# Kernel optimization log

Hardware: AMD Instinct MI355X
Metric: run time of the kernel (lower is better)

Reference implementation:

```python
import jax, jax.numpy as jnp
import numpy as np

N, NFEAT, NHID, NHEADS, NCLASS, NBLOCKS = 4096, 1024, 64, 8, 8, 3
ALPHA = 0.1       # LeakyReLU negative slope
NEG = -9e15       # mask value used by pyGAT


def setup_inputs() -> dict:
    key = jax.random.key(0)
    ks = jax.random.split(key, 8)
    x = jax.random.normal(ks[0], (N, NFEAT), jnp.float32)
    # sparse-ish symmetric adjacency with self loops (0/1 int mask)
    a = (jax.random.uniform(ks[1], (N, N)) < 0.01).astype(jnp.int32)
    adj = jnp.maximum(jnp.maximum(a, a.T), jnp.eye(N, dtype=jnp.int32))
    s = 0.1
    W_heads = (jax.random.normal(ks[2], (NHEADS, NFEAT, NHID), jnp.float32) * s)
    a_heads = (jax.random.normal(ks[3], (NHEADS, 2 * NHID), jnp.float32) * s)
    W_out = (jax.random.normal(ks[4], (NHEADS * NHID, NHID), jnp.float32) * s)
    a_out = (jax.random.normal(ks[5], (2 * NHID,), jnp.float32) * s)
    W_gcn = (jax.random.normal(ks[6], (NBLOCKS, NHID, NHID), jnp.float32) * s)
    W_cls = (jax.random.normal(ks[7], (NHID, NCLASS), jnp.float32) * s)
    return dict(x=x, adj=adj, W_heads=W_heads, a_heads=a_heads,
                W_out=W_out, a_out=a_out, W_gcn=W_gcn, W_cls=W_cls)


def _gat_layer(h, mask, W, a, concat):
    # classic pyGAT dense GraphAttentionLayer (inference: dropout off)
    Wh = h @ W                      # [N, nhid]
    nh = Wh.shape[1]
    f1 = Wh @ a[:nh]                # [N]
    f2 = Wh @ a[nh:]                # [N]
    e = jax.nn.leaky_relu(f1[:, None] + f2[None, :], ALPHA)  # [N, N]
    att = jax.nn.softmax(jnp.where(mask, e, NEG), axis=1)
    hp = att @ Wh                   # [N, nhid]
    return jax.nn.elu(hp) if concat else hp


def reference(x, adj, W_heads, a_heads, W_out, a_out, W_gcn, W_cls):
    mask = adj > 0
    # multi-head GAT, concat heads (loop over small fixed head count to keep
    # peak memory at one [N,N] score matrix per step)
    heads = [_gat_layer(x, mask, W_heads[i], a_heads[i], True)
             for i in range(NHEADS)]
    h = jnp.concatenate(heads, axis=1)           # [N, nheads*nhid]
    h = _gat_layer(h, mask, W_out, a_out, False)  # [N, nhid]
    # ModifiedGCN: symmetric-normalized dense propagation, n_blocks + head
    af = adj.astype(h.dtype)
    dinv = jax.lax.rsqrt(jnp.sum(af, axis=1))
    a_norm = af * dinv[:, None] * dinv[None, :]   # D^-1/2 A D^-1/2
    for i in range(NBLOCKS):
        h = jax.nn.relu(a_norm @ (h @ W_gcn[i]))
    return a_norm @ (h @ W_cls)                   # [N, nclass]
```

## Files before the change

### kernel.cpp

```cpp
#include <hip/hip_runtime.h>
#include <hip/hip_bf16.h>
#include <math.h>

#define N_NODES 4096
#define NFEAT   1024
#define NHEADS  8
#define ALPHA   0.1f
#define MAXDEG  256

typedef short short8 __attribute__((ext_vector_type(8)));
typedef float f32x4  __attribute__((ext_vector_type(4)));

__device__ __forceinline__ ushort f2bf(float f) {
    uint b = __float_as_uint(f);
    b += 0x7FFFu + ((b >> 16) & 1u);
    return (ushort)(b >> 16);
}
__device__ __forceinline__ float bf2f(ushort u) {
    return __uint_as_float(((uint)u) << 16);
}

__global__ __launch_bounds__(256) void prep_all(const float* __restrict__ x,
                                                const int* __restrict__ adj,
                                                const float* __restrict__ Whd,
                                                const float* __restrict__ Wo,
                                                short* __restrict__ x3,
                                                short* __restrict__ W3,
                                                short* __restrict__ W23,
                                                ushort* __restrict__ csr,
                                                int* __restrict__ rowlen,
                                                float* __restrict__ dinv) {
    __shared__ float tile[64][65];
    int b = blockIdx.x, t = threadIdx.x;
    if (b < 4096) {
        size_t idx = ((size_t)b * 256 + t) * 4;
        int row = (int)(idx >> 10);
        int col = (int)(idx & 1023);
        float4 v = *(const float4*)(x + idx);
        ushort h0 = f2bf(v.x), h1 = f2bf(v.y), h2 = f2bf(v.z), h3 = f2bf(v.w);
        short4 h = make_short4((short)h0, (short)h1, (short)h2, (short)h3);
        short4 l = make_short4((short)f2bf(v.x - bf2f(h0)), (short)f2bf(v.y - bf2f(h1)),
                               (short)f2bf(v.z - bf2f(h2)), (short)f2bf(v.w - bf2f(h3)));
        short* rp = x3 + (size_t)row * 3072 + col;
        *(short4*)(rp)        = h;
        *(short4*)(rp + 1024) = l;
        *(short4*)(rp + 2048) = h;
        return;
    }
    if (b < 4232) {
        const float* W; short* B3; int K, head, kb;
        if (b < 4224) { int id = b - 4096; W = Whd; B3 = W3;  K = 1024; head = id >> 4; kb = id & 15; }
        else          { int id = b - 4224; W = Wo;  B3 = W23; K = 512;  head = 0;       kb = id; }
        int k0 = kb * 64;
        const float* src = W + (size_t)head * K * 64 + (size_t)k0 * 64;
#pragma unroll
        for (int i = 0; i < 16; i++) {
            int lin = t + i * 256;
            int kk = lin >> 6, nn = lin & 63;
            tile[nn][kk] = src[kk * 64 + nn];
        }
        __syncthreads();
#pragma unroll
        for (int i = 0; i < 16; i++) {
            int lin = t + i * 256;
            int nn = lin >> 6, kk = lin & 63;
            float v = tile[nn][kk];
            ushort h = f2bf(v);
            ushort l = f2bf(v - bf2f(h));
            short* rp = B3 + (size_t)(head * 64 + nn) * (3 * (size_t)K) + k0 + kk;
            rp[0]     = (short)h;
            rp[K]     = (short)h;
            rp[2 * K] = (short)l;
        }
        return;
    }
    int wid = t >> 6, lane = t & 63;
    int row = (b - 4232) * 4 + wid;
    const int4* arow = (const int4*)(adj + (size_t)row * N_NODES);
    unsigned long long pre = (1ull << lane) - 1ull;
    int count = 0;
    ushort* crow = csr + (size_t)row * MAXDEG;
    for (int blk = 0; blk < N_NODES / 256; blk++) {
        int4 v = arow[blk * 64 + lane];
        unsigned long long m0 = __ballot(v.x != 0);
        unsigned long long m1 = __ballot(v.y != 0);
        unsigned long long m2 = __ballot(v.z != 0);
        unsigned long long m3 = __ballot(v.w != 0);
        int pos = count + __popcll(m0 & pre) + __popcll(m1 & pre)
                        + __popcll(m2 & pre) + __popcll(m3 & pre);
        int base = blk * 256 + lane * 4;
        if (v.x) { if (pos < MAXDEG) crow[pos] = (ushort)base;       pos++; }
        if (v.y) { if (pos < MAXDEG) crow[pos] = (ushort)(base + 1); pos++; }
        if (v.z) { if (pos < MAXDEG) crow[pos] = (ushort)(base + 2); pos++; }
        if (v.w) { if (pos < MAXDEG) crow[pos] = (ushort)(base + 3); pos++; }
        count += __popcll(m0) + __popcll(m1) + __popcll(m2) + __popcll(m3);
    }
    if (lane == 0) {
        rowlen[row] = count < MAXDEG ? count : MAXDEG;
        dinv[row] = 1.0f / sqrtf((float)count);
    }
}

#define GBM 64
#define GBN 64
#define GBK 64
#define LDK 72

__global__ __launch_bounds__(256, 2) void gemm_mfma(const short* __restrict__ A,
                                                    const short* __restrict__ B,
                                                    float* __restrict__ C,
                                                    int Kp, int kChunk, int cPartStride,
                                                    int swz, int headmajor,
                                                    const float* __restrict__ aH,
                                                    float* __restrict__ f1h,
                                                    float* __restrict__ f2h) {
    __shared__ __align__(16) short As[2][GBM * LDK];
    __shared__ __align__(16) short Bs[2][GBN * LDK];

    int tid = threadIdx.x, lane = tid & 63, wid = tid >> 6;
    int wr = wid >> 1, wc = wid & 1;
    int bx, by;
    if (swz) {
        int lin = blockIdx.x;
        bx = (lin & 7) * 8 + (lin >> 6);
        by = (lin >> 3) & 7;
    } else {
        bx = blockIdx.x; by = blockIdx.y;
    }
    int row0 = bx * GBM, col0 = by * GBN;
    int kbase = blockIdx.z * kChunk;
    C += (size_t)blockIdx.z * cPartStride;

    int aRow[2], aKc[2], bRow[2], bKc[2];
#pragma unroll
    for (int c = 0; c < 2; c++) {
        int lin = tid + c * 256;
        aRow[c] = lin >> 3; aKc[c] = (lin & 7) * 8;
        bRow[c] = lin >> 3; bKc[c] = (lin & 7) * 8;
    }

    short8 rA[2], rB[2];
    auto LOAD = [&](int k0) {
#pragma unroll
        for (int c = 0; c < 2; c++) {
            rA[c] = *(const short8*)(A + (size_t)(row0 + aRow[c]) * Kp + kbase + k0 + aKc[c]);
            rB[c] = *(const short8*)(B + (size_t)(col0 + bRow[c]) * Kp + kbase + k0 + bKc[c]);
        }
    };
    auto WRITE = [&](int buf) {
#pragma unroll
        for (int c = 0; c < 2; c++) {
            *(short8*)&As[buf][aRow[c] * LDK + aKc[c]] = rA[c];
            *(short8*)&Bs[buf][bRow[c] * LDK + bKc[c]] = rB[c];
        }
    };

    f32x4 acc[2][2];
#pragma unroll
    for (int m = 0; m < 2; m++)
#pragma unroll
        for (int n = 0; n < 2; n++) acc[m][n] = (f32x4){0.f, 0.f, 0.f, 0.f};

    LOAD(0);
    WRITE(0);
    __syncthreads();

    int nt = kChunk / GBK;
    for (int t = 0; t < nt; ++t) {
        int cur = t & 1;
        if (t + 1 < nt) LOAD((t + 1) * GBK);
#pragma unroll
        for (int ks = 0; ks < 2; ++ks) {
            short8 ah[2], bh[2];
            int ko = ks * 32 + (lane >> 4) * 8;
#pragma unroll
            for (int m = 0; m < 2; m++)
                ah[m] = *(const short8*)&As[cur][(wr * 32 + m * 16 + (lane & 15)) * LDK + ko];
#pragma unroll
            for (int n = 0; n < 2; n++)
                bh[n] = *(const short8*)&Bs[cur][(wc * 32 + n * 16 + (lane & 15)) * LDK + ko];
#pragma unroll
            for (int m = 0; m < 2; m++)
#pragma unroll
                for (int n = 0; n < 2; n++)
                    acc[m][n] = __builtin_amdgcn_mfma_f32_16x16x32_bf16(ah[m], bh[n], acc[m][n], 0, 0, 0);
        }
        if (t + 1 < nt) WRITE(cur ^ 1);
        __syncthreads();
    }

#pragma unroll
    for (int m = 0; m < 2; m++)
#pragma unroll
        for (int n = 0; n < 2; n++)
#pragma unroll
            for (int r = 0; r < 4; r++) {
                int rr = row0 + wr * 32 + m * 16 + (lane >> 4) * 4 + r;
                int cc = col0 + wc * 32 + n * 16 + (lane & 15);
                if (headmajor)
                    C[(size_t)(cc >> 6) * (N_NODES * 64) + (size_t)rr * 64 + (cc & 63)] = acc[m][n][r];
                else
                    C[(size_t)rr * 64 + cc] = acc[m][n][r];
            }

    if (aH) {
        __shared__ float f1p[2][64], f2p[2][64];
        const float* ahp = aH + by * 128;
        int cl = lane & 15;
        float a1x = ahp[wc * 32 + cl],      a1y = ahp[wc * 32 + 16 + cl];
        float a2x = ahp[64 + wc * 32 + cl], a2y = ahp[64 + wc * 32 + 16 + cl];
#pragma unroll
        for (int m = 0; m < 2; m++)
#pragma unroll
            for (int r = 0; r < 4; r++) {
                float s1 = acc[m][0][r] * a1x + acc[m][1][r] * a1y;
                float s2 = acc[m][0][r] * a2x + acc[m][1][r] * a2y;
#pragma unroll
                for (int off = 1; off < 16; off <<= 1) {
                    s1 += __shfl_xor(s1, off);
                    s2 += __shfl_xor(s2, off);
                }
                if ((lane & 15) == 0) {
                    int rl = wr * 32 + m * 16 + (lane >> 4) * 4 + r;
                    f1p[wc][rl] = s1;
                    f2p[wc][rl] = s2;
                }
            }
        __syncthreads();
        if (tid < 64) {
            f1h[(size_t)by * N_NODES + row0 + tid] = f1p[0][tid] + f1p[1][tid];
            f2h[(size_t)by * N_NODES + row0 + tid] = f2p[0][tid] + f2p[1][tid];
        }
    }
}

__global__ __launch_bounds__(512, 8) void attn1(const float* __restrict__ Whh,
                                                const float* __restrict__ f1h,
                                                const float* __restrict__ f2h,
                                                const ushort* __restrict__ csr,
                                                const int* __restrict__ rowlen,
                                                short* __restrict__ hp3) {
    __shared__ float  f2s[N_NODES];
    __shared__ float  w[8][MAXDEG];
    __shared__ ushort cols[8][MAXDEG];
    int lin = blockIdx.x;
    int h = lin & 7;
    int wid = threadIdx.x >> 6, lane = threadIdx.x & 63;
    int i = (lin >> 3) * 8 + wid;

    {
        const float4* f2g = (const float4*)(f2h + (size_t)h * N_NODES);
        float4 v0 = f2g[threadIdx.x];
        float4 v1 = f2g[threadIdx.x + 512];
        *(float4*)&f2s[threadIdx.x * 4] = v0;
        *(float4*)&f2s[(threadIdx.x + 512) * 4] = v1;
    }
    __syncthreads();

    int len = rowlen[i];
    const ushort* crow = csr + (size_t)i * MAXDEG;
    float f1v = f1h[(size_t)h * N_NODES + i];

    float ev[4]; int cv[4];
    float m = -1e30f;
#pragma unroll
    for (int c = 0; c < 4; c++) {
        int k = lane + c * 64;
        if (k < len) {
            int j = crow[k];
            float e = f1v + f2s[j];
            e = e > 0.f ? e : ALPHA * e;
            ev[c] = e; cv[c] = j;
            m = fmaxf(m, e);
        }
    }
#pragma unroll
    for (int off = 32; off; off >>= 1) m = fmaxf(m, __shfl_xor(m, off));
    float s = 0.f;
#pragma unroll
    for (int c = 0; c < 4; c++) {
        int k = lane + c * 64;
        if (k < len) {
            float ex = __expf(ev[c] - m);
            s += ex;
            w[wid][k] = ex;
            cols[wid][k] = (ushort)cv[c];
        }
    }
#pragma unroll
    for (int off = 32; off; off >>= 1) s += __shfl_xor(s, off);
    float sinv = 1.0f / s;

    int len16 = (len + 15) & ~15;
    if (lane < len16 - len) {
        w[wid][len + lane] = 0.f;
        cols[wid][len + lane] = 0;
    }

    int q = lane >> 4, d = lane & 15;
    const float4* base = (const float4*)(Whh + (size_t)h * (N_NODES * 64)) + d;
    f32x4 A0 = {0.f,0.f,0.f,0.f}, A1 = A0, A2 = A0, A3 = A0;
    for (int k = 0; k < len16; k += 16) {
        int   j0 = cols[wid][k + q];       float w0 = w[wid][k + q];
        int   j1 = cols[wid][k + 4 + q];   float w1 = w[wid][k + 4 + q];
        int   j2 = cols[wid][k + 8 + q];   float w2 = w[wid][k + 8 + q];
        int   j3 = cols[wid][k + 12 + q];  float w3 = w[wid][k + 12 + q];
        float4 v0 = base[(size_t)j0 * 16];
        float4 v1 = base[(size_t)j1 * 16];
        float4 v2 = base[(size_t)j2 * 16];
        float4 v3 = base[(size_t)j3 * 16];
        A0[0] += w0 * v0.x; A0[1] += w0 * v0.y; A0[2] += w0 * v0.z; A0[3] += w0 * v0.w;
        A1[0] += w1 * v1.x; A1[1] += w1 * v1.y; A1[2] += w1 * v1.z; A1[3] += w1 * v1.w;
        A2[0] += w2 * v2.x; A2[1] += w2 * v2.y; A2[2] += w2 * v2.z; A2[3] += w2 * v2.w;
        A3[0] += w3 * v3.x; A3[1] += w3 * v3.y; A3[2] += w3 * v3.z; A3[3] += w3 * v3.w;
    }
    float rx = (A0[0] + A1[0]) + (A2[0] + A3[0]);
    float ry = (A0[1] + A1[1]) + (A2[1] + A3[1]);
    float rz = (A0[2] + A1[2]) + (A2[2] + A3[2]);
    float rw = (A0[3] + A1[3]) + (A2[3] + A3[3]);
#pragma unroll
    for (int off = 16; off <= 32; off <<= 1) {
        rx += __shfl_xor(rx, off);
        ry += __shfl_xor(ry, off);
        rz += __shfl_xor(rz, off);
        rw += __shfl_xor(rw, off);
    }
    if (lane < 16) {
        float v[4] = {rx * sinv, ry * sinv, rz * sinv, rw * sinv};
        short hi[4], lo[4];
#pragma unroll
        for (int c = 0; c < 4; c++) {
            float e = v[c] > 0.f ? v[c] : __expf(v[c]) - 1.f;
            ushort hh = f2bf(e);
            hi[c] = (short)hh;
            lo[c] = (short)f2bf(e - bf2f(hh));
        }
        short* rp = hp3 + (size_t)i * 1536 + h * 64 + d * 4;
        *(short4*)(rp)        = make_short4(hi[0], hi[1], hi[2], hi[3]);
        *(short4*)(rp + 512)  = make_short4(lo[0], lo[1], lo[2], lo[3]);
        *(short4*)(rp + 1024) = make_short4(hi[0], hi[1], hi[2], hi[3]);
    }
}

__global__ __launch_bounds__(256) void f2sum(const float* __restrict__ part,
                                             const float* __restrict__ a,
                                             float* __restrict__ Wh2,
                                             float* __restrict__ f1o,
                                             float* __restrict__ f2o) {
    int wid = threadIdx.x >> 6, l = threadIdx.x & 63;
    int i = blockIdx.x * 4 + wid;
    size_t o = (size_t)i * 64 + l;
    const size_t S = (size_t)N_NODES * 64;
    float v = part[o] + part[o + S] + part[o + 2 * S] + part[o + 3 * S];
    Wh2[o] = v;
    float p1 = v * a[l], p2 = v * a[64 + l];
#pragma unroll
    for (int off = 32; off; off >>= 1) {
        p1 += __shfl_xor(p1, off);
        p2 += __shfl_xor(p2, off);
    }
    if (l == 0) { f1o[i] = p1; f2o[i] = p2; }
}

__global__ __launch_bounds__(256, 6) void attn2_g0(const float* __restrict__ Wh2,
                                                   const float* __restrict__ f1o,
                                                   const float* __restrict__ f2o,
                                                   const ushort* __restrict__ csr,
                                                   const int* __restrict__ rowlen,
                                                   const float* __restrict__ W0,
                                                   const float* __restrict__ dinv,
                                                   float* __restrict__ t0) {
    __shared__ float  f2s[N_NODES];
    __shared__ float  w[4][MAXDEG];
    __shared__ ushort cl[4][MAXDEG];
    __shared__ float  hrow[4][64];
    int wid = threadIdx.x >> 6, lane = threadIdx.x & 63;
    int i = blockIdx.x * 4 + wid;

    {
        const float4* f2g = (const float4*)f2o;
#pragma unroll
        for (int c = 0; c < 4; c++) {
            int idx = threadIdx.x + c * 256;
            *(float4*)&f2s[idx * 4] = f2g[idx];
        }
    }
    __syncthreads();

    int len = rowlen[i];
    const ushort* crow = csr + (size_t)i * MAXDEG;
    float myf1 = f1o[i];

    float ev[4]; int cv[4];
    float m = -1e30f;
#pragma unroll
    for (int c = 0; c < 4; c++) {
        int k = lane + c * 64;
        if (k < len) {
            int j = crow[k];
            float e = myf1 + f2s[j];
            e = e > 0.f ? e : ALPHA * e;
            ev[c] = e; cv[c] = j;
            m = fmaxf(m, e);
        }
    }
#pragma unroll
    for (int off = 32; off; off >>= 1) m = fmaxf(m, __shfl_xor(m, off));
    float s = 0.f;
#pragma unroll
    for (int c = 0; c < 4; c++) {
        int k = lane + c * 64;
        if (k < len) {
            float ex = __expf(ev[c] - m);
            s += ex;
            w[wid][k] = ex;
            cl[wid][k] = (ushort)cv[c];
        }
    }
#pragma unroll
    for (int off = 32; off; off >>= 1) s += __shfl_xor(s, off);
    float sinv = 1.0f / s;

    int len16 = (len + 15) & ~15;
    if (lane < len16 - len) {
        w[wid][len + lane] = 0.f;
        cl[wid][len + lane] = 0;
    }

    int q = lane >> 4, d = lane & 15;
    const float4* base = (const float4*)Wh2 + d;
    f32x4 A0 = {0.f,0.f,0.f,0.f}, A1 = A0, A2 = A0, A3 = A0;
    for (int k = 0; k < len16; k += 16) {
        int   j0 = cl[wid][k + q];       float w0 = w[wid][k + q];
        int   j1 = cl[wid][k + 4 + q];   float w1 = w[wid][k + 4 + q];
        int   j2 = cl[wid][k + 8 + q];   float w2 = w[wid][k + 8 + q];
        int   j3 = cl[wid][k + 12 + q];  float w3 = w[wid][k + 12 + q];
        float4 v0 = base[(size_t)j0 * 16];
        float4 v1 = base[(size_t)j1 * 16];
        float4 v2 = base[(size_t)j2 * 16];
        float4 v3 = base[(size_t)j3 * 16];
        A0[0] += w0 * v0.x; A0[1] += w0 * v0.y; A0[2] += w0 * v0.z; A0[3] += w0 * v0.w;
        A1[0] += w1 * v1.x; A1[1] += w1 * v1.y; A1[2] += w1 * v1.z; A1[3] += w1 * v1.w;
        A2[0] += w2 * v2.x; A2[1] += w2 * v2.y; A2[2] += w2 * v2.z; A2[3] += w2 * v2.w;
        A3[0] += w3 * v3.x; A3[1] += w3 * v3.y; A3[2] += w3 * v3.z; A3[3] += w3 * v3.w;
    }
    float rx = (A0[0] + A1[0]) + (A2[0] + A3[0]);
    float ry = (A0[1] + A1[1]) + (A2[1] + A3[1]);
    float rz = (A0[2] + A1[2]) + (A2[2] + A3[2]);
    float rw = (A0[3] + A1[3]) + (A2[3] + A3[3]);
#pragma unroll
    for (int off = 16; off <= 32; off <<= 1) {
        rx += __shfl_xor(rx, off);
        ry += __shfl_xor(ry, off);
        rz += __shfl_xor(rz, off);
        rw += __shfl_xor(rw, off);
    }
    if (lane < 16) {
        float4 r = make_float4(rx * sinv, ry * sinv, rz * sinv, rw * sinv);
        *(float4*)&hrow[wid][d * 4] = r;
    }

    float ox = 0.f, oy = 0.f, oz = 0.f, ow = 0.f;
#pragma unroll
    for (int it = 0; it < 16; it++) {
        int kk = q * 16 + it;
        float hv = hrow[wid][kk];
        float4 wv = *(const float4*)(W0 + kk * 64 + d * 4);
        ox += hv * wv.x; oy += hv * wv.y; oz += hv * wv.z; ow += hv * wv.w;
    }
#pragma unroll
    for (int off = 16; off <= 32; off <<= 1) {
        ox += __shfl_xor(ox, off);
        oy += __shfl_xor(oy, off);
        oz += __shfl_xor(oz, off);
        ow += __shfl_xor(ow, off);
    }
    if (lane < 16) {
        float di = dinv[i];
        *(float4*)(t0 + (size_t)i * 64 + d * 4) =
            make_float4(ox * di, oy * di, oz * di, ow * di);
    }
}

__global__ __launch_bounds__(256, 4) void spmv_gemm(const float* __restrict__ t,
                                                    const ushort* __restrict__ csr,
                                                    const int* __restrict__ rowlen,
                                                    const float* __restrict__ W,
                                                    const float* __restrict__ dinv,
                                                    float* __restrict__ out) {
    __shared__ float hrow[4][64];
    int wid = threadIdx.x >> 6, lane = threadIdx.x & 63;
    int i = blockIdx.x * 4 + wid;
    int len = rowlen[i];
    const ushort* ci = csr + (size_t)i * MAXDEG;
    int q = lane >> 4, d = lane & 15;
    const float4* base = (const float4*)t + d;
    int len16 = (len + 15) & ~15;
    f32x4 A0 = {0.f,0.f,0.f,0.f}, A1 = A0, A2 = A0, A3 = A0;
    for (int k = 0; k < len16; k += 16) {
        int k0 = k + q, k1 = k + 4 + q, k2 = k + 8 + q, k3 = k + 12 + q;
        float m0 = k0 < len ? 1.f : 0.f;
        float m1 = k1 < len ? 1.f : 0.f;
        float m2 = k2 < len ? 1.f : 0.f;
        float m3 = k3 < len ? 1.f : 0.f;
        int j0 = ci[k0 < len ? k0 : 0];
        int j1 = ci[k1 < len ? k1 : 0];
        int j2 = ci[k2 < len ? k2 : 0];
        int j3 = ci[k3 < len ? k3 : 0];
        float4 v0 = base[(size_t)j0 * 16];
        float4 v1 = base[(size_t)j1 * 16];
        float4 v2 = base[(size_t)j2 * 16];
        float4 v3 = base[(size_t)j3 * 16];
        A0[0] += m0 * v0.x; A0[1] += m0 * v0.y; A0[2] += m0 * v0.z; A0[3] += m0 * v0.w;
        A1[0] += m1 * v1.x; A1[1] += m1 * v1.y; A1[2] += m1 * v1.z; A1[3] += m1 * v1.w;
        A2[0] += m2 * v2.x; A2[1] += m2 * v2.y; A2[2] += m2 * v2.z; A2[3] += m2 * v2.w;
        A3[0] += m3 * v3.x; A3[1] += m3 * v3.y; A3[2] += m3 * v3.z; A3[3] += m3 * v3.w;
    }
    float rx = (A0[0] + A1[0]) + (A2[0] + A3[0]);
    float ry = (A0[1] + A1[1]) + (A2[1] + A3[1]);
    float rz = (A0[2] + A1[2]) + (A2[2] + A3[2]);
    float rw = (A0[3] + A1[3]) + (A2[3] + A3[3]);
#pragma unroll
    for (int off = 16; off <= 32; off <<= 1) {
        rx += __shfl_xor(rx, off);
        ry += __shfl_xor(ry, off);
        rz += __shfl_xor(rz, off);
        rw += __shfl_xor(rw, off);
    }
    float di = dinv[i];
    if (lane < 16) {
        float4 r = make_float4(fmaxf(rx * di, 0.f), fmaxf(ry * di, 0.f),
                               fmaxf(rz * di, 0.f), fmaxf(rw * di, 0.f));
        *(float4*)&hrow[wid][d * 4] = r;
    }

    float ox = 0.f, oy = 0.f, oz = 0.f, ow = 0.f;
#pragma unroll
    for (int it = 0; it < 16; it++) {
        int kk = q * 16 + it;
        float hv = hrow[wid][kk];
        float4 wv = *(const float4*)(W + kk * 64 + d * 4);
        ox += hv * wv.x; oy += hv * wv.y; oz += hv * wv.z; ow += hv * wv.w;
    }
#pragma unroll
    for (int off = 16; off <= 32; off <<= 1) {
        ox += __shfl_xor(ox, off);
        oy += __shfl_xor(oy, off);
        oz += __shfl_xor(oz, off);
        ow += __shfl_xor(ow, off);
    }
    if (lane < 16)
        *(float4*)(out + (size_t)i * 64 + d * 4) =
            make_float4(ox * di, oy * di, oz * di, ow * di);
}

__global__ __launch_bounds__(256, 4) void spmv_cls(const float* __restrict__ t,
                                                   const ushort* __restrict__ csr,
                                                   const int* __restrict__ rowlen,
                                                   const float* __restrict__ Wc,
                                                   const float* __restrict__ dinv,
                                                   float* __restrict__ t8) {
    __shared__ float hrow[4][64];
    int wid = threadIdx.x >> 6, lane = threadIdx.x & 63;
    int i = blockIdx.x * 4 + wid;
    int len = rowlen[i];
    const ushort* ci = csr + (size_t)i * MAXDEG;
    int q = lane >> 4, d = lane & 15;
    const float4* base = (const float4*)t + d;
    int len16 = (len + 15) & ~15;
    f32x4 A0 = {0.f,0.f,0.f,0.f}, A1 = A0, A2 = A0, A3 = A0;
    for (int k = 0; k < len16; k += 16) {
        int k0 = k + q, k1 = k + 4 + q, k2 = k + 8 + q, k3 = k + 12 + q;
        float m0 = k0 < len ? 1.f : 0.f;
        float m1 = k1 < len ? 1.f : 0.f;
        float m2 = k2 < len ? 1.f : 0.f;
        float m3 = k3 < len ? 1.f : 0.f;
        int j0 = ci[k0 < len ? k0 : 0];
        int j1 = ci[k1 < len ? k1 : 0];
        int j2 = ci[k2 < len ? k2 : 0];
        int j3 = ci[k3 < len ? k3 : 0];
        float4 v0 = base[(size_t)j0 * 16];
        float4 v1 = base[(size_t)j1 * 16];
        float4 v2 = base[(size_t)j2 * 16];
        float4 v3 = base[(size_t)j3 * 16];
        A0[0] += m0 * v0.x; A0[1] += m0 * v0.y; A0[2] += m0 * v0.z; A0[3] += m0 * v0.w;
        A1[0] += m1 * v1.x; A1[1] += m1 * v1.y; A1[2] += m1 * v1.z; A1[3] += m1 * v1.w;
        A2[0] += m2 * v2.x; A2[1] += m2 * v2.y; A2[2] += m2 * v2.z; A2[3] += m2 * v2.w;
        A3[0] += m3 * v3.x; A3[1] += m3 * v3.y; A3[2] += m3 * v3.z; A3[3] += m3 * v3.w;
    }
    float rx = (A0[0] + A1[0]) + (A2[0] + A3[0]);
    float ry = (A0[1] + A1[1]) + (A2[1] + A3[1]);
    float rz = (A0[2] + A1[2]) + (A2[2] + A3[2]);
    float rw = (A0[3] + A1[3]) + (A2[3] + A3[3]);
#pragma unroll
    for (int off = 16; off <= 32; off <<= 1) {
        rx += __shfl_xor(rx, off);
        ry += __shfl_xor(ry, off);
        rz += __shfl_xor(rz, off);
        rw += __shfl_xor(rw, off);
    }
    float di = dinv[i];
    if (lane < 16) {
        float4 r = make_float4(fmaxf(rx * di, 0.f), fmaxf(ry * di, 0.f),
                               fmaxf(rz * di, 0.f), fmaxf(rw * di, 0.f));
        *(float4*)&hrow[wid][d * 4] = r;
    }
    int col = lane & 7, k0s = (lane >> 3) * 8;
    float o = 0.f;
#pragma unroll
    for (int kk = 0; kk < 8; kk++) o += hrow[wid][k0s + kk] * Wc[(k0s + kk) * 8 + col];
    o += __shfl_down(o, 32);
    o += __shfl_down(o, 16);
    o += __shfl_down(o, 8);
    if (lane < 8) t8[(size_t)i * 8 + lane] = o * di;
}

__global__ __launch_bounds__(256) void spmv8(const float* __restrict__ t8,
                                             const ushort* __restrict__ csr,
                                             const int* __restrict__ rowlen,
                                             const float* __restrict__ dinv,
                                             float* __restrict__ out) {
    int wid = threadIdx.x >> 6, lane = threadIdx.x & 63;
    int i = blockIdx.x * 4 + wid;
    int len = rowlen[i];
    const ushort* ci = csr + (size_t)i * MAXDEG;
    int col = lane & 7, chunk = lane >> 3;
    float acc = 0.f;
    for (int k = chunk; k < len; k += 8)
        acc += t8[(size_t)ci[k] * 8 + col];
    acc += __shfl_down(acc, 32);
    acc += __shfl_down(acc, 16);
    acc += __shfl_down(acc, 8);
    if (lane < 8) out[(size_t)i * 8 + lane] = acc * dinv[i];
}

extern "C" void kernel_launch(void* const* d_in, const int* in_sizes, int n_in,
                              void* d_out, int out_size, void* d_ws, size_t ws_size,
                              hipStream_t stream) {
    const float* x       = (const float*)d_in[0];
    const int*   adj     = (const int*)d_in[1];
    const float* W_heads = (const float*)d_in[2];
    const float* a_heads = (const float*)d_in[3];
    const float* W_out   = (const float*)d_in[4];
    const float* a_out   = (const float*)d_in[5];
    const float* W_gcn   = (const float*)d_in[6];
    const float* W_cls   = (const float*)d_in[7];
    float* outp = (float*)d_out;

    char* p = (char*)d_ws;
    short*  x3     = (short*)p;  p += (size_t)N_NODES * 3072 * 2;
    short*  W3     = (short*)p;  p += (size_t)512 * 3072 * 2;
    short*  W23    = (short*)p;  p += (size_t)64 * 1536 * 2;
    float*  Whh    = (float*)p;  p += (size_t)NHEADS * N_NODES * 64 * 4;
    float*  f1h    = (float*)p;  p += (size_t)NHEADS * N_NODES * 4;
    float*  f2h    = (float*)p;  p += (size_t)NHEADS * N_NODES * 4;
    float*  Wh2    = (float*)p;  p += (size_t)N_NODES * 64 * 4;
    float*  f1o    = (float*)p;  p += (size_t)N_NODES * 4;
    float*  f2o    = (float*)p;  p += (size_t)N_NODES * 4;
    float*  tA     = (float*)p;  p += (size_t)N_NODES * 64 * 4;
    float*  tB     = (float*)p;  p += (size_t)N_NODES * 64 * 4;
    float*  t8     = (float*)p;  p += (size_t)N_NODES * 8 * 4;
    float*  dinv   = (float*)p;  p += (size_t)N_NODES * 4;
    int*    rowlen = (int*)p;    p += (size_t)N_NODES * 4;
    ushort* csr    = (ushort*)p; p += (size_t)N_NODES * MAXDEG * 2;

    short* hp3  = x3;
    float* part = (float*)((char*)x3 + (16u << 20));

    prep_all<<<4096 + 128 + 8 + 1024, 256, 0, stream>>>(
        x, adj, W_heads, W_out, x3, W3, W23, csr, rowlen, dinv);

    gemm_mfma<<<512, 256, 0, stream>>>(x3, W3, Whh, 3072, 3072, 0, 1, 1,
                                       a_heads, f1h, f2h);

    attn1<<<N_NODES * NHEADS / 8, 512, 0, stream>>>(Whh, f1h, f2h, csr, rowlen, hp3);

    gemm_mfma<<<dim3(N_NODES / GBM, 1, 4), 256, 0, stream>>>(
        hp3, W23, part, 1536, 384, N_NODES * 64, 0, 0, nullptr, nullptr, nullptr);

    f2sum<<<N_NODES / 4, 256, 0, stream>>>(part, a_out, Wh2, f1o, f2o);

    attn2_g0<<<N_NODES / 4, 256, 0, stream>>>(Wh2, f1o, f2o, csr, rowlen, W_gcn, dinv, tA);

    spmv_gemm<<<N_NODES / 4, 256, 0, stream>>>(tA, csr, rowlen, W_gcn + 4096, dinv, tB);
    spmv_gemm<<<N_NODES / 4, 256, 0, stream>>>(tB, csr, rowlen, W_gcn + 8192, dinv, tA);

    spmv_cls<<<N_NODES / 4, 256, 0, stream>>>(tA, csr, rowlen, W_cls, dinv, t8);
    spmv8<<<N_NODES / 4, 256, 0, stream>>>(t8, csr, rowlen, dinv, outp);
}
```

Measured before the change: 245.1 us.

## Split bf16 hi/lo operands into separate arrays and issue three MFMAs per tile

Instead of materialising a tripled [h,l,h] concatenated K dimension for the split-bf16 GEMMs, the prep kernel now writes separate hi and lo arrays, and the GEMM loads both halves into separate LDS tiles and issues three MFMAs (hh, hl, lh) per fragment. This removes the duplicated hi copy in global memory and the extra write/read traffic, at the cost of doubled LDS footprint per block. attn1 now processes two rows per wave with an 8-wide gather loop, writing separate hp_h/hp_l outputs. spmv_gemm launch bounds are raised for occupancy.

```diff
diff --git a/kernel.cpp b/kernel.cpp
--- a/kernel.cpp
+++ b/kernel.cpp
@@ -24,9 +24,12 @@
                                                 const int* __restrict__ adj,
                                                 const float* __restrict__ Whd,
                                                 const float* __restrict__ Wo,
-                                                short* __restrict__ x3,
-                                                short* __restrict__ W3,
-                                                short* __restrict__ W23,
+                                                short* __restrict__ x_h,
+                                                short* __restrict__ x_l,
+                                                short* __restrict__ W3h,
+                                                short* __restrict__ W3l,
+                                                short* __restrict__ W2h,
+                                                short* __restrict__ W2l,
                                                 ushort* __restrict__ csr,
                                                 int* __restrict__ rowlen,
                                                 float* __restrict__ dinv) {
@@ -34,23 +37,19 @@
     int b = blockIdx.x, t = threadIdx.x;
     if (b < 4096) {
         size_t idx = ((size_t)b * 256 + t) * 4;
-        int row = (int)(idx >> 10);
-        int col = (int)(idx & 1023);
         float4 v = *(const float4*)(x + idx);
         ushort h0 = f2bf(v.x), h1 = f2bf(v.y), h2 = f2bf(v.z), h3 = f2bf(v.w);
         short4 h = make_short4((short)h0, (short)h1, (short)h2, (short)h3);
         short4 l = make_short4((short)f2bf(v.x - bf2f(h0)), (short)f2bf(v.y - bf2f(h1)),
                                (short)f2bf(v.z - bf2f(h2)), (short)f2bf(v.w - bf2f(h3)));
-        short* rp = x3 + (size_t)row * 3072 + col;
-        *(short4*)(rp)        = h;
-        *(short4*)(rp + 1024) = l;
-        *(short4*)(rp + 2048) = h;
+        *(short4*)(x_h + idx) = h;
+        *(short4*)(x_l + idx) = l;
         return;
     }
     if (b < 4232) {
-        const float* W; short* B3; int K, head, kb;
-        if (b < 4224) { int id = b - 4096; W = Whd; B3 = W3;  K = 1024; head = id >> 4; kb = id & 15; }
-        else          { int id = b - 4224; W = Wo;  B3 = W23; K = 512;  head = 0;       kb = id; }
+        const float* W; short* Bh; short* Bl; int K, head, kb;
+        if (b < 4224) { int id = b - 4096; W = Whd; Bh = W3h; Bl = W3l; K = 1024; head = id >> 4; kb = id & 15; }
+        else          { int id = b - 4224; W = Wo;  Bh = W2h; Bl = W2l; K = 512;  head = 0;       kb = id; }
         int k0 = kb * 64;
         const float* src = W + (size_t)head * K * 64 + (size_t)k0 * 64;
 #pragma unroll
@@ -67,10 +66,9 @@
             float v = tile[nn][kk];
             ushort h = f2bf(v);
             ushort l = f2bf(v - bf2f(h));
-            short* rp = B3 + (size_t)(head * 64 + nn) * (3 * (size_t)K) + k0 + kk;
-            rp[0]     = (short)h;
-            rp[K]     = (short)h;
-            rp[2 * K] = (short)l;
+            size_t o = (size_t)(head * 64 + nn) * K + k0 + kk;
+            Bh[o] = (short)h;
+            Bl[o] = (short)l;
         }
         return;
     }
@@ -106,16 +104,20 @@
 #define GBK 64
 #define LDK 72
 
-__global__ __launch_bounds__(256, 2) void gemm_mfma(const short* __restrict__ A,
-                                                    const short* __restrict__ B,
-                                                    float* __restrict__ C,
-                                                    int Kp, int kChunk, int cPartStride,
-                                                    int swz, int headmajor,
-                                                    const float* __restrict__ aH,
-                                                    float* __restrict__ f1h,
-                                                    float* __restrict__ f2h) {
-    __shared__ __align__(16) short As[2][GBM * LDK];
-    __shared__ __align__(16) short Bs[2][GBN * LDK];
+__global__ __launch_bounds__(256, 2) void gemm3(const short* __restrict__ Ah,
+                                                const short* __restrict__ Al,
+                                                const short* __restrict__ Bh,
+                                                const short* __restrict__ Bl,
+                                                float* __restrict__ C,
+                                                int Kp, int kChunk, int cPartStride,
+                                                int swz, int headmajor,
+                                                const float* __restrict__ aH,
+                                                float* __restrict__ f1h,
+                                                float* __restrict__ f2h) {
+    __shared__ __align__(16) short Ash[2][GBM * LDK];
+    __shared__ __align__(16) short Asl[2][GBM * LDK];
+    __shared__ __align__(16) short Bsh[2][GBN * LDK];
+    __shared__ __align__(16) short Bsl[2][GBN * LDK];
 
     int tid = threadIdx.x, lane = tid & 63, wid = tid >> 6;
     int wr = wid >> 1, wc = wid & 1;
@@ -131,27 +133,33 @@
     int kbase = blockIdx.z * kChunk;
     C += (size_t)blockIdx.z * cPartStride;
 
-    int aRow[2], aKc[2], bRow[2], bKc[2];
+    int aRow[2], aKc[2];
 #pragma unroll
     for (int c = 0; c < 2; c++) {
         int lin = tid + c * 256;
         aRow[c] = lin >> 3; aKc[c] = (lin & 7) * 8;
-        bRow[c] = lin >> 3; bKc[c] = (lin & 7) * 8;
-    }
-
-    short8 rA[2], rB[2];
+    }
+
+    short8 rAh[2], rAl[2], rBh[2], rBl[2];
     auto LOAD = [&](int k0) {
 #pragma unroll
         for (int c = 0; c < 2; c++) {
-            rA[c] = *(const short8*)(A + (size_t)(row0 + aRow[c]) * Kp + kbase + k0 + aKc[c]);
-            rB[c] = *(const short8*)(B + (size_t)(col0 + bRow[c]) * Kp + kbase + k0 + bKc[c]);
+            size_t ga = (size_t)(row0 + aRow[c]) * Kp + kbase + k0 + aKc[c];
+            size_t gb = (size_t)(col0 + aRow[c]) * Kp + kbase + k0 + aKc[c];
+            rAh[c] = *(const short8*)(Ah + ga);
+            rAl[c] = *(const short8*)(Al + ga);
+            rBh[c] = *(const short8*)(Bh + gb);
+            rBl[c] = *(const short8*)(Bl + gb);
         }
     };
     auto WRITE = [&](int buf) {
 #pragma unroll
         for (int c = 0; c < 2; c++) {
-            *(short8*)&As[buf][aRow[c] * LDK + aKc[c]] = rA[c];
-            *(short8*)&Bs[buf][bRow[c] * LDK + bKc[c]] = rB[c];
+            int o = aRow[c] * LDK + aKc[c];
+            *(short8*)&Ash[buf][o] = rAh[c];
+            *(short8*)&Asl[buf][o] = rAl[c];
+            *(short8*)&Bsh[buf][o] = rBh[c];
+            *(short8*)&Bsl[buf][o] = rBl[c];
         }
     };
 
@@ -171,19 +179,28 @@
         if (t + 1 < nt) LOAD((t + 1) * GBK);
 #pragma unroll
         for (int ks = 0; ks < 2; ++ks) {
-            short8 ah[2], bh[2];
+            short8 ah[2], al[2], bh[2], bl[2];
             int ko = ks * 32 + (lane >> 4) * 8;
 #pragma unroll
+            for (int m = 0; m < 2; m++) {
+                int r = (wr * 32 + m * 16 + (lane & 15)) * LDK + ko;
+                ah[m] = *(const short8*)&Ash[cur][r];
+                al[m] = *(const short8*)&Asl[cur][r];
+            }
+#pragma unroll
+            for (int n = 0; n < 2; n++) {
+                int r = (wc * 32 + n * 16 + (lane & 15)) * LDK + ko;
+                bh[n] = *(const short8*)&Bsh[cur][r];
+                bl[n] = *(const short8*)&Bsl[cur][r];
+            }
+#pragma unroll
             for (int m = 0; m < 2; m++)
-                ah[m] = *(const short8*)&As[cur][(wr * 32 + m * 16 + (lane & 15)) * LDK + ko];
-#pragma unroll
-            for (int n = 0; n < 2; n++)
-                bh[n] = *(const short8*)&Bs[cur][(wc * 32 + n * 16 + (lane & 15)) * LDK + ko];
-#pragma unroll
-            for (int m = 0; m < 2; m++)
-#pragma unroll
-                for (int n = 0; n < 2; n++)
+#pragma unroll
+                for (int n = 0; n < 2; n++) {
                     acc[m][n] = __builtin_amdgcn_mfma_f32_16x16x32_bf16(ah[m], bh[n], acc[m][n], 0, 0, 0);
+                    acc[m][n] = __builtin_amdgcn_mfma_f32_16x16x32_bf16(ah[m], bl[n], acc[m][n], 0, 0, 0);
+                    acc[m][n] = __builtin_amdgcn_mfma_f32_16x16x32_bf16(al[m], bh[n], acc[m][n], 0, 0, 0);
+                }
         }
         if (t + 1 < nt) WRITE(cur ^ 1);
         __syncthreads();
@@ -234,19 +251,21 @@
     }
 }
 
-__global__ __launch_bounds__(512, 8) void attn1(const float* __restrict__ Whh,
+__global__ __launch_bounds__(512, 4) void attn1(const float* __restrict__ Whh,
                                                 const float* __restrict__ f1h,
                                                 const float* __restrict__ f2h,
                                                 const ushort* __restrict__ csr,
                                                 const int* __restrict__ rowlen,
-                                                short* __restrict__ hp3) {
+                                                short* __restrict__ hp_h,
+                                                short* __restrict__ hp_l) {
     __shared__ float  f2s[N_NODES];
-    __shared__ float  w[8][MAXDEG];
-    __shared__ ushort cols[8][MAXDEG];
+    __shared__ float  w[16][MAXDEG];
+    __shared__ ushort cols[16][MAXDEG];
     int lin = blockIdx.x;
     int h = lin & 7;
     int wid = threadIdx.x >> 6, lane = threadIdx.x & 63;
-    int i = (lin >> 3) * 8 + wid;
+    int i0 = (lin >> 3) * 16 + wid * 2;
+    int sA = wid * 2, sB = sA + 1;
 
     {
         const float4* f2g = (const float4*)(f2h + (size_t)h * N_NODES);
@@ -257,88 +276,96 @@
     }
     __syncthreads();
 
-    int len = rowlen[i];
-    const ushort* crow = csr + (size_t)i * MAXDEG;
-    float f1v = f1h[(size_t)h * N_NODES + i];
-
-    float ev[4]; int cv[4];
-    float m = -1e30f;
-#pragma unroll
-    for (int c = 0; c < 4; c++) {
-        int k = lane + c * 64;
-        if (k < len) {
-            int j = crow[k];
-            float e = f1v + f2s[j];
-            e = e > 0.f ? e : ALPHA * e;
-            ev[c] = e; cv[c] = j;
-            m = fmaxf(m, e);
-        }
-    }
-#pragma unroll
-    for (int off = 32; off; off >>= 1) m = fmaxf(m, __shfl_xor(m, off));
-    float s = 0.f;
-#pragma unroll
-    for (int c = 0; c < 4; c++) {
-        int k = lane + c * 64;
-        if (k < len) {
-            float ex = __expf(ev[c] - m);
-            s += ex;
-            w[wid][k] = ex;
-            cols[wid][k] = (ushort)cv[c];
-        }
-    }
-#pragma unroll
-    for (int off = 32; off; off >>= 1) s += __shfl_xor(s, off);
-    float sinv = 1.0f / s;
-
-    int len16 = (len + 15) & ~15;
-    if (lane < len16 - len) {
-        w[wid][len + lane] = 0.f;
-        cols[wid][len + lane] = 0;
-    }
+    float sinvR[2];
+    int lenR[2];
+#pragma unroll
+    for (int r = 0; r < 2; r++) {
+        int i = i0 + r, slot = sA + r;
+        int len = rowlen[i];
+        lenR[r] = len;
+        const ushort* crow = csr + (size_t)i * MAXDEG;
+        float f1v = f1h[(size_t)h * N_NODES + i];
+        float ev[4]; int cv[4];
+        float m = -1e30f;
+#pragma unroll
+        for (int c = 0; c < 4; c++) {
+            int k = lane + c * 64;
+            if (k < len) {
+                int j = crow[k];
+                float e = f1v + f2s[j];
+                e = e > 0.f ? e : ALPHA * e;
+                ev[c] = e; cv[c] = j;
+                m = fmaxf(m, e);
+            }
+        }
+#pragma unroll
+        for (int off = 32; off; off >>= 1) m = fmaxf(m, __shfl_xor(m, off));
+        float s = 0.f;
+#pragma unroll
+        for (int c = 0; c < 4; c++) {
+            int k = lane + c * 64;
+            if (k < len) {
+                float ex = __expf(ev[c] - m);
+                s += ex;
+                w[slot][k] = ex;
+                cols[slot][k] = (ushort)cv[c];
+            }
+        }
+#pragma unroll
+        for (int off = 32; off; off >>= 1) s += __shfl_xor(s, off);
+        sinvR[r] = 1.0f / s;
+    }
+
+    int lc = lenR[0] > lenR[1] ? lenR[0] : lenR[1];
+    int len8 = (lc + 7) & ~7;
+    for (int k = lenR[0] + lane; k < len8; k += 64) { w[sA][k] = 0.f; cols[sA][k] = 0; }
+    for (int k = lenR[1] + lane; k < len8; k += 64) { w[sB][k] = 0.f; cols[sB][k] = 0; }
 
     int q = lane >> 4, d = lane & 15;
     const float4* base = (const float4*)(Whh + (size_t)h * (N_NODES * 64)) + d;
-    f32x4 A0 = {0.f,0.f,0.f,0.f}, A1 = A0, A2 = A0, A3 = A0;
-    for (int k = 0; k < len16; k += 16) {
-        int   j0 = cols[wid][k + q];       float w0 = w[wid][k + q];
-        int   j1 = cols[wid][k + 4 + q];   float w1 = w[wid][k + 4 + q];
-        int   j2 = cols[wid][k + 8 + q];   float w2 = w[wid][k + 8 + q];
-        int   j3 = cols[wid][k + 12 + q];  float w3 = w[wid][k + 12 + q];
-        float4 v0 = base[(size_t)j0 * 16];
-        float4 v1 = base[(size_t)j1 * 16];
-        float4 v2 = base[(size_t)j2 * 16];
-        float4 v3 = base[(size_t)j3 * 16];
-        A0[0] += w0 * v0.x; A0[1] += w0 * v0.y; A0[2] += w0 * v0.z; A0[3] += w0 * v0.w;
-        A1[0] += w1 * v1.x; A1[1] += w1 * v1.y; A1[2] += w1 * v1.z; A1[3] += w1 * v1.w;
-        A2[0] += w2 * v2.x; A2[1] += w2 * v2.y; A2[2] += w2 * v2.z; A2[3] += w2 * v2.w;
-        A3[0] += w3 * v3.x; A3[1] += w3 * v3.y; A3[2] += w3 * v3.z; A3[3] += w3 * v3.w;
-    }
-    float rx = (A0[0] + A1[0]) + (A2[0] + A3[0]);
-    float ry = (A0[1] + A1[1]) + (A2[1] + A3[1]);
-    float rz = (A0[2] + A1[2]) + (A2[2] + A3[2]);
-    float rw = (A0[3] + A1[3]) + (A2[3] + A3[3]);
-#pragma unroll
-    for (int off = 16; off <= 32; off <<= 1) {
-        rx += __shfl_xor(rx, off);
-        ry += __shfl_xor(ry, off);
-        rz += __shfl_xor(rz, off);
-        rw += __shfl_xor(rw, off);
-    }
-    if (lane < 16) {
-        float v[4] = {rx * sinv, ry * sinv, rz * sinv, rw * sinv};
-        short hi[4], lo[4];
-#pragma unroll
-        for (int c = 0; c < 4; c++) {
-            float e = v[c] > 0.f ? v[c] : __expf(v[c]) - 1.f;
-            ushort hh = f2bf(e);
-            hi[c] = (short)hh;
-            lo[c] = (short)f2bf(e - bf2f(hh));
-        }
-        short* rp = hp3 + (size_t)i * 1536 + h * 64 + d * 4;
-        *(short4*)(rp)        = make_short4(hi[0], hi[1], hi[2], hi[3]);
-        *(short4*)(rp + 512)  = make_short4(lo[0], lo[1], lo[2], lo[3]);
-        *(short4*)(rp + 1024) = make_short4(hi[0], hi[1], hi[2], hi[3]);
+    f32x4 A0 = {0.f,0.f,0.f,0.f}, A1 = A0, B0 = A0, B1 = A0;
+    for (int k = 0; k < len8; k += 8) {
+        int   ja0 = cols[sA][k + q];      float wa0 = w[sA][k + q];
+        int   ja1 = cols[sA][k + 4 + q];  float wa1 = w[sA][k + 4 + q];
+        int   jb0 = cols[sB][k + q];      float wb0 = w[sB][k + q];
+        int   jb1 = cols[sB][k + 4 + q];  float wb1 = w[sB][k + 4 + q];
+        float4 va0 = base[(size_t)ja0 * 16];
+        float4 va1 = base[(size_t)ja1 * 16];
+        float4 vb0 = base[(size_t)jb0 * 16];
+        float4 vb1 = base[(size_t)jb1 * 16];
+        A0[0] += wa0 * va0.x; A0[1] += wa0 * va0.y; A0[2] += wa0 * va0.z; A0[3] += wa0 * va0.w;
+        A1[0] += wa1 * va1.x; A1[1] += wa1 * va1.y; A1[2] += wa1 * va1.z; A1[3] += wa1 * va1.w;
+        B0[0] += wb0 * vb0.x; B0[1] += wb0 * vb0.y; B0[2] += wb0 * vb0.z; B0[3] += wb0 * vb0.w;
+        B1[0] += wb1 * vb1.x; B1[1] += wb1 * vb1.y; B1[2] += wb1 * vb1.z; B1[3] += wb1 * vb1.w;
+    }
+
+#pragma unroll
+    for (int r = 0; r < 2; r++) {
+        float rx, ry, rz, rw;
+        if (r == 0) { rx=A0[0]+A1[0]; ry=A0[1]+A1[1]; rz=A0[2]+A1[2]; rw=A0[3]+A1[3]; }
+        else        { rx=B0[0]+B1[0]; ry=B0[1]+B1[1]; rz=B0[2]+B1[2]; rw=B0[3]+B1[3]; }
+#pragma unroll
+        for (int off = 16; off <= 32; off <<= 1) {
+            rx += __shfl_xor(rx, off);
+            ry += __shfl_xor(ry, off);
+            rz += __shfl_xor(rz, off);
+            rw += __shfl_xor(rw, off);
+        }
+        if (lane < 16) {
+            float sinv = sinvR[r];
+            float v[4] = {rx * sinv, ry * sinv, rz * sinv, rw * sinv};
+            short hi[4], lo[4];
+#pragma unroll
+            for (int c = 0; c < 4; c++) {
+                float e = v[c] > 0.f ? v[c] : __expf(v[c]) - 1.f;
+                ushort hh = f2bf(e);
+                hi[c] = (short)hh;
+                lo[c] = (short)f2bf(e - bf2f(hh));
+            }
+            size_t o = (size_t)(i0 + r) * 512 + h * 64 + d * 4;
+            *(short4*)(hp_h + o) = make_short4(hi[0], hi[1], hi[2], hi[3]);
+            *(short4*)(hp_l + o) = make_short4(lo[0], lo[1], lo[2], lo[3]);
+        }
     }
 }
 
@@ -482,7 +509,7 @@
     }
 }
 
-__global__ __launch_bounds__(256, 4) void spmv_gemm(const float* __restrict__ t,
+__global__ __launch_bounds__(256, 6) void spmv_gemm(const float* __restrict__ t,
                                                     const ushort* __restrict__ csr,
                                                     const int* __restrict__ rowlen,
                                                     const float* __restrict__ W,
@@ -648,9 +675,12 @@
     float* outp = (float*)d_out;
 
     char* p = (char*)d_ws;
-    short*  x3     = (short*)p;  p += (size_t)N_NODES * 3072 * 2;
-    short*  W3     = (short*)p;  p += (size_t)512 * 3072 * 2;
-    short*  W23    = (short*)p;  p += (size_t)64 * 1536 * 2;
+    short*  x_h    = (short*)p;  p += (size_t)N_NODES * NFEAT * 2;
+    short*  x_l    = (short*)p;  p += (size_t)N_NODES * NFEAT * 2;
+    short*  W3h    = (short*)p;  p += (size_t)512 * NFEAT * 2;
+    short*  W3l    = (short*)p;  p += (size_t)512 * NFEAT * 2;
+    short*  W2h    = (short*)p;  p += (size_t)64 * 512 * 2;
+    short*  W2l    = (short*)p;  p += (size_t)64 * 512 * 2;
     float*  Whh    = (float*)p;  p += (size_t)NHEADS * N_NODES * 64 * 4;
     float*  f1h    = (float*)p;  p += (size_t)NHEADS * N_NODES * 4;
     float*  f2h    = (float*)p;  p += (size_t)NHEADS * N_NODES * 4;
@@ -664,19 +694,22 @@
     int*    rowlen = (int*)p;    p += (size_t)N_NODES * 4;
     ushort* csr    = (ushort*)p; p += (size_t)N_NODES * MAXDEG * 2;
 
-    short* hp3  = x3;
-    float* part = (float*)((char*)x3 + (16u << 20));
+    short* hp_h = x_h;
+    short* hp_l = x_l;
+    float* part = (float*)((char*)x_h + (4u << 20));
 
     prep_all<<<4096 + 128 + 8 + 1024, 256, 0, stream>>>(
-        x, adj, W_heads, W_out, x3, W3, W23, csr, rowlen, dinv);
-
-    gemm_mfma<<<512, 256, 0, stream>>>(x3, W3, Whh, 3072, 3072, 0, 1, 1,
-                                       a_heads, f1h, f2h);
-
-    attn1<<<N_NODES * NHEADS / 8, 512, 0, stream>>>(Whh, f1h, f2h, csr, rowlen, hp3);
-
-    gemm_mfma<<<dim3(N_NODES / GBM, 1, 4), 256, 0, stream>>>(
-        hp3, W23, part, 1536, 384, N_NODES * 64, 0, 0, nullptr, nullptr, nullptr);
+        x, adj, W_heads, W_out, x_h, x_l, W3h, W3l, W2h, W2l, csr, rowlen, dinv);
+
+    gemm3<<<512, 256, 0, stream>>>(x_h, x_l, W3h, W3l, Whh, NFEAT, NFEAT, 0,
+                                   1, 1, a_heads, f1h, f2h);
+
+    attn1<<<N_NODES * NHEADS / 16, 512, 0, stream>>>(Whh, f1h, f2h, csr, rowlen,
+                                                     hp_h, hp_l);
+
+    gemm3<<<dim3(N_NODES / GBM, 1, 4), 256, 0, stream>>>(
+        hp_h, hp_l, W2h, W2l, part, 512, 128, N_NODES * 64,
+        0, 0, nullptr, nullptr, nullptr);
 
     f2sum<<<N_NODES / 4, 256, 0, stream>>>(part, a_out, Wh2, f1o, f2o);
 
```

Measured after the change: 234.4 us. -4.4%, faster.
